# Kernel optimization log

Measured on AMD Instinct MI355X. Metric: run time of the kernel, lower is better.

## Reference

```python
import jax, jax.numpy as jnp
import numpy as np

B, S, D = 2, 2048, 1024
H, DQK = 16, 64          # n_head, d_qk = d_O // n_head
DV = 64                  # d_v = d_O // n_head
TEMP = DQK ** 0.5
EPS = 1e-6


def relu15(x):
    # ReLU capped at 15 (custom non-softmax attention activation)
    return jnp.clip(x, 0.0, 15.0)


def setup_inputs() -> dict:
    key = jax.random.key(0)
    ks = jax.random.split(key, 10)
    s = 0.02
    return {
        "q": jax.random.normal(ks[0], (B, S, D), jnp.float32),
        "k": jax.random.normal(ks[1], (B, S, D), jnp.float32),
        "v": jax.random.normal(ks[2], (B, S, D), jnp.float32),
        "Wq": jax.random.normal(ks[3], (D, H * DQK), jnp.float32) * s,
        "Wk": jax.random.normal(ks[4], (D, H * DQK), jnp.float32) * s,
        "Wv": jax.random.normal(ks[5], (D, H * DV), jnp.float32) * s,
        "Wfc": jax.random.normal(ks[6], (H * DV, H * DV), jnp.float32) * s,
        "gamma": jnp.ones((H * DV,), jnp.float32),
        "beta": jnp.zeros((H * DV,), jnp.float32),
    }


def reference(q, k, v, Wq, Wk, Wv, Wfc, gamma, beta):
    residual = q                                   # d_Q == d_O path
    # QKV projections (no bias)
    qh = (q @ Wq).reshape(B, S, H, DQK).transpose(0, 2, 1, 3)   # [B,H,S,dqk]
    kh = (k @ Wk).reshape(B, S, H, DQK).transpose(0, 2, 1, 3)
    vh = (v @ Wv).reshape(B, S, H, DV).transpose(0, 2, 1, 3)
    # custom attention: scaled scores -> ReLU15 (no softmax normalization)
    attn = jnp.einsum('bhqd,bhkd->bhqk', qh / TEMP, kh)          # [B,H,S,S]
    attn = relu15(attn)
    o = jnp.einsum('bhqk,bhkd->bhqd', attn, vh)                  # [B,H,S,dv]
    o = o.transpose(0, 2, 1, 3).reshape(B, S, H * DV)            # [B,S,d_O]
    # output projection + residual + LayerNorm
    o = o @ Wfc + residual
    mu = jnp.mean(o, axis=-1, keepdims=True)
    var = jnp.var(o, axis=-1, keepdims=True)
    o = (o - mu) / jnp.sqrt(var + EPS) * gamma + beta
    return o
```

## Files before the change

### kernel.cpp

```cpp
#include <hip/hip_runtime.h>
#include <stdint.h>

#define DEV static __device__ __forceinline__

typedef __attribute__((ext_vector_type(4)))  float f32x4;
typedef __attribute__((ext_vector_type(16))) float f32x16;
typedef __bf16 bf16x8 __attribute__((ext_vector_type(8)));

constexpr int Bc = 2, S = 2048, Dm = 1024, H = 16, DH = 64;
constexpr int BS  = Bc * S;
constexpr int HSZ = Bc * H * S * DH;

constexpr size_t OFF_QKVB  = 0;
constexpr size_t OFF_WT    = 25165824;
constexpr size_t OFF_HEADS = 33554432;
constexpr size_t OFF_VT    = 58720256;
constexpr size_t OFF_O     = 67108864;

DEV uint16_t f2bf(float f) {
    uint32_t u = __float_as_uint(f);
    uint32_t r = u + 0x7FFFu + ((u >> 16) & 1u);
    return (uint16_t)(r >> 16);
}
DEV uint32_t cvtpk(float lo, float hi) {
    uint32_t r;
    asm("v_cvt_pk_bf16_f32 %0, %1, %2" : "=v"(r) : "v"(lo), "v"(hi));
    return r;
}
DEV float clip15(float x, float c15) {
    float r;
    asm("v_med3_f32 %0, %1, 0, %2" : "=v"(r) : "v"(x), "v"(c15));
    return r;
}
DEV uint32_t swz128(uint32_t byteoff) {
    return byteoff ^ (((byteoff >> 7) & 7u) << 4);
}
DEV void gll16(const void* g, void* l) {
    auto gp = (const __attribute__((address_space(1))) uint32_t*)g;
    auto lp = (__attribute__((address_space(3))) uint32_t*)l;
    __builtin_amdgcn_global_load_lds(gp, lp, 16, 0, 0);
}
DEV bf16x8 ld_frag(const char* base, uint32_t logical_off) {
    return __builtin_bit_cast(bf16x8, *(const uint4*)(base + swz128(logical_off)));
}
DEV bf16x8 ld_frag_g(const void* p) {
    return __builtin_bit_cast(bf16x8, *(const uint4*)p);
}

__global__ __launch_bounds__(256) void k_convert(const float* __restrict__ q,
                                                 const float* __restrict__ k,
                                                 const float* __restrict__ v,
                                                 uint16_t* __restrict__ out) {
    const int64_t n1 = (int64_t)BS * Dm;
    int64_t i = ((int64_t)blockIdx.x * 256 + threadIdx.x) * 8;
    const float* src; int64_t j;
    if (i < n1)            { src = q; j = i; }
    else if (i < 2 * n1)   { src = k; j = i - n1; }
    else                   { src = v; j = i - 2 * n1; }
    float4 a = *(const float4*)(src + j);
    float4 b = *(const float4*)(src + j + 4);
    union { uint16_t u[8]; uint4 q4; } o;
    o.u[0] = f2bf(a.x); o.u[1] = f2bf(a.y); o.u[2] = f2bf(a.z); o.u[3] = f2bf(a.w);
    o.u[4] = f2bf(b.x); o.u[5] = f2bf(b.y); o.u[6] = f2bf(b.z); o.u[7] = f2bf(b.w);
    *(uint4*)(out + i) = o.q4;
}

__global__ __launch_bounds__(256) void k_transw(const float* __restrict__ w0,
                                                const float* __restrict__ w1,
                                                const float* __restrict__ w2,
                                                const float* __restrict__ w3,
                                                uint16_t* __restrict__ wt) {
    int mat = blockIdx.y;
    const float* w = (mat == 0) ? w0 : (mat == 1) ? w1 : (mat == 2) ? w2 : w3;
    float scale = (mat == 0) ? 0.125f : 1.0f;
    uint16_t* out = wt + (size_t)mat * 1024 * 1024;
    int tile = blockIdx.x;
    int tr = (tile >> 4) << 6, tc = (tile & 15) << 6;
    __shared__ float lds[64][65];
    int t = threadIdx.x;
#pragma unroll
    for (int p = 0; p < 4; ++p) {
        int r = p * 16 + (t >> 4);
        int c = (t & 15) * 4;
        float4 x = *(const float4*)(w + (size_t)(tr + r) * 1024 + tc + c);
        lds[r][c] = x.x; lds[r][c + 1] = x.y; lds[r][c + 2] = x.z; lds[r][c + 3] = x.w;
    }
    __syncthreads();
    int n = t >> 2, kc = (t & 3) * 16;
    union { uint16_t u[16]; uint4 q[2]; } tt;
#pragma unroll
    for (int j = 0; j < 16; ++j) tt.u[j] = f2bf(lds[kc + j][n] * scale);
    uint16_t* dst = out + (size_t)(tc + n) * 1024 + tr + kc;
    *(uint4*)dst = tt.q[0];
    *(uint4*)(dst + 8) = tt.q[1];
}

struct Acc { f32x4 a[4][4]; };

DEV void stage128(const uint16_t* g, int ldbytes, char* lds) {
    int tid = threadIdx.x;
#pragma unroll
    for (int it = 0; it < 4; ++it) {
        uint32_t p = it * 4096 + tid * 16;
        uint32_t lo = swz128(p);
        uint32_t row = lo >> 7, col = lo & 127;
        gll16((const char*)g + (size_t)row * ldbytes + col,
              lds + it * 4096 + (tid & ~63) * 16);
    }
}

DEV void gemm_core(const uint16_t* Ta, const uint16_t* Tb, int K,
                   char* la, char* lb, Acc& acc) {
    int lane = threadIdx.x & 63, w = threadIdx.x >> 6;
    int wr = w >> 1, wc = w & 1;
#pragma unroll
    for (int ia = 0; ia < 4; ++ia)
#pragma unroll
        for (int ib = 0; ib < 4; ++ib)
#pragma unroll
            for (int r = 0; r < 4; ++r) acc.a[ia][ib][r] = 0.f;
    for (int k0 = 0; k0 < K; k0 += 64) {
        __syncthreads();
        stage128(Ta + k0, K * 2, la);
        stage128(Tb + k0, K * 2, lb);
        __syncthreads();
#pragma unroll
        for (int kk = 0; kk < 2; ++kk) {
            bf16x8 af[4], bfr[4];
#pragma unroll
            for (int ia = 0; ia < 4; ++ia) {
                uint32_t row = wr * 64 + ia * 16 + (lane & 15);
                af[ia] = ld_frag(la, row * 128 + kk * 64 + (lane >> 4) * 16);
            }
#pragma unroll
            for (int ib = 0; ib < 4; ++ib) {
                uint32_t row = wc * 64 + ib * 16 + (lane & 15);
                bfr[ib] = ld_frag(lb, row * 128 + kk * 64 + (lane >> 4) * 16);
            }
#pragma unroll
            for (int ia = 0; ia < 4; ++ia)
#pragma unroll
                for (int ib = 0; ib < 4; ++ib)
                    acc.a[ia][ib] = __builtin_amdgcn_mfma_f32_16x16x32_bf16(
                        af[ia], bfr[ib], acc.a[ia][ib], 0, 0, 0);
        }
    }
}

__global__ __launch_bounds__(256) void k_proj(const uint16_t* __restrict__ qkvb,
                                              const uint16_t* __restrict__ WT,
                                              uint16_t* __restrict__ heads) {
    __shared__ char lds[32768];
    int raw = blockIdx.x;
    int blk = (raw & 7) * 96 + (raw >> 3);
    int sel = blk >> 8;
    int t2 = blk & 255; int bm = t2 >> 3, bn = t2 & 7;
    const uint16_t* Act = qkvb + (size_t)sel * BS * Dm + (size_t)bm * 128 * Dm;
    const uint16_t* Wtt = WT   + (size_t)sel * Dm * Dm + (size_t)bn * 128 * Dm;
    Acc acc;
    gemm_core(Wtt, Act, 1024, lds, lds + 16384, acc);
    uint16_t* out = heads + (size_t)sel * HSZ;
    int lane = threadIdx.x & 63, w = threadIdx.x >> 6;
    int na = bn * 128 + (w >> 1) * 64, mb = bm * 128 + (w & 1) * 64;
#pragma unroll
    for (int ia = 0; ia < 4; ++ia)
#pragma unroll
        for (int ib = 0; ib < 4; ++ib) {
            int n0 = na + ia * 16 + (lane >> 4) * 4;
            int m  = mb + ib * 16 + (lane & 15);
            uint2 d;
            d.x = cvtpk(acc.a[ia][ib][0], acc.a[ia][ib][1]);
            d.y = cvtpk(acc.a[ia][ib][2], acc.a[ia][ib][3]);
            int b = m >> 11, s = m & 2047, h = n0 >> 6, dd = n0 & 63;
            *(uint2*)(out + (((size_t)(b * H + h)) * S + s) * 64 + dd) = d;
        }
}

__global__ __launch_bounds__(256) void k_transv(const uint16_t* __restrict__ Vh,
                                                uint16_t* __restrict__ Vt) {
    int bh = blockIdx.x >> 5, st = blockIdx.x & 31;
    int s0 = st * 64;
    const uint16_t* src = Vh + (size_t)bh * S * 64 + (size_t)s0 * 64;
    uint16_t* dst = Vt + (size_t)bh * 64 * S;
    __shared__ uint16_t lds[64][65];
    int t = threadIdx.x;
    {
        int r = t >> 2, c = (t & 3) * 16;
        union { uint16_t u[16]; uint4 q[2]; } x;
        x.q[0] = *(const uint4*)(src + (size_t)r * 64 + c);
        x.q[1] = *(const uint4*)(src + (size_t)r * 64 + c + 8);
#pragma unroll
        for (int j = 0; j < 16; ++j) lds[r][c + j] = x.u[j];
    }
    __syncthreads();
    {
        int d = t >> 2, sc = (t & 3) * 16;
        union { uint16_t u[16]; uint4 q[2]; } x;
#pragma unroll
        for (int j = 0; j < 16; ++j) x.u[j] = lds[sc + j][d];
        uint16_t* p = dst + (size_t)d * S + s0 + sc;
        *(uint4*)p = x.q[0];
        *(uint4*)(p + 8) = x.q[1];
    }
}

__global__ __launch_bounds__(128) void k_attn(const uint16_t* __restrict__ Qh,
                                              const uint16_t* __restrict__ Kh,
                                              const uint16_t* __restrict__ Vt,
                                              uint16_t* __restrict__ O) {
    __shared__ char kbuf[2][8192];
    __shared__ char vbuf[2][8192];
    int raw = blockIdx.x;
    int bid = (raw & 7) * 64 + (raw >> 3);
    int bh = bid >> 4, qb = (bid & 15) * 128;
    int tid = threadIdx.x, lane = tid & 63, w = tid >> 6;
    int l31 = lane & 31, hi = lane >> 5;
    const char* Kbase = (const char*)(Kh + (size_t)bh * S * 64);
    const char* Vbase = (const char*)(Vt + (size_t)bh * 64 * S);

    bf16x8 qf[2][4];
#pragma unroll
    for (int qs = 0; qs < 2; ++qs) {
        const char* qrow = (const char*)(Qh + (size_t)bh * S * 64
                                         + (size_t)(qb + w * 64 + qs * 32 + l31) * 64);
#pragma unroll
        for (int ks = 0; ks < 4; ++ks)
            qf[qs][ks] = ld_frag_g(qrow + ks * 32 + hi * 16);
    }
    f32x16 oa[2][2];
#pragma unroll
    for (int qs = 0; qs < 2; ++qs)
#pragma unroll
        for (int nt = 0; nt < 2; ++nt)
#pragma unroll
            for (int r = 0; r < 16; ++r) oa[qs][nt][r] = 0.f;
    float c15 = 15.0f;

    auto stageKV = [&](int tile, int bufi) {
        int kv0 = tile * 64;
#pragma unroll
        for (int it = 0; it < 4; ++it) {
            uint32_t p = it * 2048 + tid * 16;
            uint32_t lo = swz128(p);
            uint32_t row = lo >> 7, col = lo & 127;
            gll16(Kbase + (size_t)(kv0 + row) * 128 + col,
                  kbuf[bufi] + it * 2048 + (tid & ~63) * 16);
            gll16(Vbase + (size_t)row * 4096 + (size_t)kv0 * 2 + col,
                  vbuf[bufi] + it * 2048 + (tid & ~63) * 16);
        }
    };

    stageKV(0, 0);
    __syncthreads();
    for (int t = 0; t < 32; ++t) {
        int cur = t & 1;
        if (t < 31) stageKV(t + 1, cur ^ 1);
        __builtin_amdgcn_s_setprio(1);
#pragma unroll
        for (int mt = 0; mt < 2; ++mt) {
            bf16x8 kf[4];
#pragma unroll
            for (int ks = 0; ks < 4; ++ks)
                kf[ks] = ld_frag(kbuf[cur], (mt * 32 + l31) * 128 + ks * 32 + hi * 16);
            bf16x8 pa[2][2];
#pragma unroll
            for (int qs = 0; qs < 2; ++qs) {
                f32x16 c;
#pragma unroll
                for (int r = 0; r < 16; ++r) c[r] = 0.f;
#pragma unroll
                for (int ks = 0; ks < 4; ++ks)
                    c = __builtin_amdgcn_mfma_f32_32x32x16_bf16(kf[ks], qf[qs][ks], c, 0, 0, 0);
#pragma unroll
                for (int r = 0; r < 16; ++r) c[r] = clip15(c[r], c15);
#pragma unroll
                for (int ks2 = 0; ks2 < 2; ++ks2) {
                    union { uint32_t w[4]; bf16x8 v; } up;
#pragma unroll
                    for (int jj = 0; jj < 2; ++jj) {
                        uint32_t sA = cvtpk(c[8 * ks2 + 2 * jj],     c[8 * ks2 + 2 * jj + 1]);
                        uint32_t sB = cvtpk(c[8 * ks2 + 4 + 2 * jj], c[8 * ks2 + 4 + 2 * jj + 1]);
                        asm volatile("v_permlane32_swap_b32 %0, %1" : "+v"(sA), "+v"(sB));
                        up.w[jj] = sA; up.w[2 + jj] = sB;
                    }
                    pa[qs][ks2] = up.v;
                }
            }
#pragma unroll
            for (int ks2 = 0; ks2 < 2; ++ks2)
#pragma unroll
                for (int nt = 0; nt < 2; ++nt) {
                    bf16x8 vb = ld_frag(vbuf[cur],
                                        (nt * 32 + l31) * 128 + mt * 64 + ks2 * 32 + hi * 16);
#pragma unroll
                    for (int qs = 0; qs < 2; ++qs)
                        oa[qs][nt] = __builtin_amdgcn_mfma_f32_32x32x16_bf16(
                            vb, pa[qs][ks2], oa[qs][nt], 0, 0, 0);
                }
        }
        __builtin_amdgcn_s_setprio(0);
        __syncthreads();
    }
    int b = bh >> 4, h = bh & 15;
#pragma unroll
    for (int qs = 0; qs < 2; ++qs) {
        int q = qb + w * 64 + qs * 32 + l31;
#pragma unroll
        for (int nt = 0; nt < 2; ++nt)
#pragma unroll
            for (int g = 0; g < 4; ++g) {
                uint2 d;
                d.x = cvtpk(oa[qs][nt][4 * g],     oa[qs][nt][4 * g + 1]);
                d.y = cvtpk(oa[qs][nt][4 * g + 2], oa[qs][nt][4 * g + 3]);
                int col = h * 64 + nt * 32 + 8 * g + 4 * hi;
                *(uint2*)(O + ((size_t)(b * S + q)) * 1024 + col) = d;
            }
    }
}

__global__ __launch_bounds__(256) void k_fc(const uint16_t* __restrict__ Ob,
                                            const uint16_t* __restrict__ WfcT,
                                            const float* __restrict__ resid,
                                            float* __restrict__ out) {
    __shared__ char lds[32768];
    int raw = blockIdx.x;
    int blk = (raw & 7) * 32 + (raw >> 3);
    int bm = blk >> 3, bn = blk & 7;
    const uint16_t* Act = Ob   + (size_t)bm * 128 * Dm;
    const uint16_t* Wtt = WfcT + (size_t)bn * 128 * Dm;
    Acc acc;
    gemm_core(Wtt, Act, 1024, lds, lds + 16384, acc);
    int lane = threadIdx.x & 63, w = threadIdx.x >> 6;
    int na = bn * 128 + (w >> 1) * 64, mb = bm * 128 + (w & 1) * 64;
#pragma unroll
    for (int ia = 0; ia < 4; ++ia)
#pragma unroll
        for (int ib = 0; ib < 4; ++ib) {
            int n0 = na + ia * 16 + (lane >> 4) * 4;
            int m  = mb + ib * 16 + (lane & 15);
            size_t idx = (size_t)m * 1024 + n0;
            float4 r4 = *(const float4*)(resid + idx);
            float4 o;
            o.x = acc.a[ia][ib][0] + r4.x;
            o.y = acc.a[ia][ib][1] + r4.y;
            o.z = acc.a[ia][ib][2] + r4.z;
            o.w = acc.a[ia][ib][3] + r4.w;
            *(float4*)(out + idx) = o;
        }
}

__global__ __launch_bounds__(256) void k_ln(float* __restrict__ io,
                                            const float* __restrict__ gamma,
                                            const float* __restrict__ beta) {
    int row = blockIdx.x;
    float* p = io + (size_t)row * 1024;
    int t = threadIdx.x;
    float4 x = *(const float4*)(p + t * 4);
    float s  = x.x + x.y + x.z + x.w;
    float s2 = x.x * x.x + x.y * x.y + x.z * x.z + x.w * x.w;
#pragma unroll
    for (int o = 32; o > 0; o >>= 1) { s += __shfl_xor(s, o); s2 += __shfl_xor(s2, o); }
    __shared__ float red[8];
    int w = t >> 6, lane = t & 63;
    if (lane == 0) { red[w] = s; red[4 + w] = s2; }
    __syncthreads();
    s  = red[0] + red[1] + red[2] + red[3];
    s2 = red[4] + red[5] + red[6] + red[7];
    float mu  = s * (1.f / 1024.f);
    float var = s2 * (1.f / 1024.f) - mu * mu;
    float inv = rsqrtf(var + 1e-6f);
    float4 g  = *(const float4*)(gamma + t * 4);
    float4 bb = *(const float4*)(beta + t * 4);
    x.x = (x.x - mu) * inv * g.x + bb.x;
    x.y = (x.y - mu) * inv * g.y + bb.y;
    x.z = (x.z - mu) * inv * g.z + bb.z;
    x.w = (x.w - mu) * inv * g.w + bb.w;
    *(float4*)(p + t * 4) = x;
}

extern "C" void kernel_launch(void* const* d_in, const int* in_sizes, int n_in,
                              void* d_out, int out_size, void* d_ws, size_t ws_size,
                              hipStream_t stream) {
    (void)in_sizes; (void)n_in; (void)out_size; (void)ws_size;
    const float* q     = (const float*)d_in[0];
    const float* k     = (const float*)d_in[1];
    const float* v     = (const float*)d_in[2];
    const float* Wq    = (const float*)d_in[3];
    const float* Wk    = (const float*)d_in[4];
    const float* Wv    = (const float*)d_in[5];
    const float* Wfc   = (const float*)d_in[6];
    const float* gamma = (const float*)d_in[7];
    const float* beta  = (const float*)d_in[8];
    char* ws = (char*)d_ws;
    uint16_t* qkvb  = (uint16_t*)(ws + OFF_QKVB);
    uint16_t* WT    = (uint16_t*)(ws + OFF_WT);
    uint16_t* heads = (uint16_t*)(ws + OFF_HEADS);
    uint16_t* Vt    = (uint16_t*)(ws + OFF_VT);
    uint16_t* Ob    = (uint16_t*)(ws + OFF_O);
    float* out = (float*)d_out;

    k_convert<<<dim3(6144), dim3(256), 0, stream>>>(q, k, v, qkvb);
    k_transw <<<dim3(256, 4), dim3(256), 0, stream>>>(Wq, Wk, Wv, Wfc, WT);
    k_proj   <<<dim3(768), dim3(256), 0, stream>>>(qkvb, WT, heads);
    k_transv <<<dim3(1024), dim3(256), 0, stream>>>(heads + 2 * (size_t)HSZ, Vt);
    k_attn   <<<dim3(512), dim3(128), 0, stream>>>(heads, heads + HSZ, Vt, Ob);
    k_fc     <<<dim3(256), dim3(256), 0, stream>>>(Ob, WT + 3 * 1024 * 1024, q, out);
    k_ln     <<<dim3(4096), dim3(256), 0, stream>>>(out, gamma, beta);
}
```

Measured before the change: 258.7 us.

## Triple-buffer K/V tiles in attention with explicit vmcnt waits and single barrier

Replaces the double-buffered K/V LDS staging with a three-slot ring, prefetching two tiles ahead. Each iteration waits on vmcnt for only the oldest tile's loads, then issues one raw s_barrier instead of a full __syncthreads at the end of the loop. The aim is to overlap global-to-LDS loads more deeply with MFMA work and cut synchronization stalls. It raises LDS use from 32KB to 48KB per block, which may lower occupancy, and it relies on the hand-counted vmcnt value being correct.

```diff
diff --git a/kernel.cpp b/kernel.cpp
--- a/kernel.cpp
+++ b/kernel.cpp
@@ -208,8 +208,7 @@
                                               const uint16_t* __restrict__ Kh,
                                               const uint16_t* __restrict__ Vt,
                                               uint16_t* __restrict__ O) {
-    __shared__ char kbuf[2][8192];
-    __shared__ char vbuf[2][8192];
+    __shared__ char kv[3][16384];
     int raw = blockIdx.x;
     int bid = (raw & 7) * 64 + (raw >> 3);
     int bh = bid >> 4, qb = (bid & 15) * 128;
@@ -236,7 +235,8 @@
             for (int r = 0; r < 16; ++r) oa[qs][nt][r] = 0.f;
     float c15 = 15.0f;
 
-    auto stageKV = [&](int tile, int bufi) {
+    auto stageKV = [&](int tile) {
+        int bufi = tile % 3;
         int kv0 = tile * 64;
 #pragma unroll
         for (int it = 0; it < 4; ++it) {
@@ -244,24 +244,29 @@
             uint32_t lo = swz128(p);
             uint32_t row = lo >> 7, col = lo & 127;
             gll16(Kbase + (size_t)(kv0 + row) * 128 + col,
-                  kbuf[bufi] + it * 2048 + (tid & ~63) * 16);
+                  kv[bufi] + it * 2048 + (tid & ~63) * 16);
             gll16(Vbase + (size_t)row * 4096 + (size_t)kv0 * 2 + col,
-                  vbuf[bufi] + it * 2048 + (tid & ~63) * 16);
+                  kv[bufi] + 8192 + it * 2048 + (tid & ~63) * 16);
         }
     };
 
-    stageKV(0, 0);
-    __syncthreads();
+    stageKV(0);
+    stageKV(1);
     for (int t = 0; t < 32; ++t) {
-        int cur = t & 1;
-        if (t < 31) stageKV(t + 1, cur ^ 1);
+        if (t < 31) { asm volatile("s_waitcnt vmcnt(8)" ::: "memory"); }
+        else        { asm volatile("s_waitcnt vmcnt(0)" ::: "memory"); }
+        __builtin_amdgcn_sched_barrier(0);
+        __builtin_amdgcn_s_barrier();
+        const char* kb = kv[t % 3];
+        const char* vb = kv[t % 3] + 8192;
+        if (t < 30) stageKV(t + 2);
         __builtin_amdgcn_s_setprio(1);
 #pragma unroll
         for (int mt = 0; mt < 2; ++mt) {
             bf16x8 kf[4];
 #pragma unroll
             for (int ks = 0; ks < 4; ++ks)
-                kf[ks] = ld_frag(kbuf[cur], (mt * 32 + l31) * 128 + ks * 32 + hi * 16);
+                kf[ks] = ld_frag(kb, (mt * 32 + l31) * 128 + ks * 32 + hi * 16);
             bf16x8 pa[2][2];
 #pragma unroll
             for (int qs = 0; qs < 2; ++qs) {
@@ -290,16 +295,14 @@
             for (int ks2 = 0; ks2 < 2; ++ks2)
 #pragma unroll
                 for (int nt = 0; nt < 2; ++nt) {
-                    bf16x8 vb = ld_frag(vbuf[cur],
-                                        (nt * 32 + l31) * 128 + mt * 64 + ks2 * 32 + hi * 16);
+                    bf16x8 vbf = ld_frag(vb, (nt * 32 + l31) * 128 + mt * 64 + ks2 * 32 + hi * 16);
 #pragma unroll
                     for (int qs = 0; qs < 2; ++qs)
                         oa[qs][nt] = __builtin_amdgcn_mfma_f32_32x32x16_bf16(
-                            vb, pa[qs][ks2], oa[qs][nt], 0, 0, 0);
+                            vbf, pa[qs][ks2], oa[qs][nt], 0, 0, 0);
                 }
         }
         __builtin_amdgcn_s_setprio(0);
-        __syncthreads();
     }
     int b = bh >> 4, h = bh & 15;
 #pragma unroll
```

Result: faster. 252.0 us (-2.6%).
